# Kernel tuning notes

Hardware: AMD Instinct MI355X
Metric: run time of the kernel (lower is better)

## Reference

```python
import jax, jax.numpy as jnp
import numpy as np

# Per-channel block sizes (init arg). [0,1] rows are identity channels.
BLOCK_SIZES = np.array(
    [[0, 1]] * 2 + [[1, 1]] * 2 + [[2, 2]] * 4 + [[4, 4]] * 4 + [[3, 3]] * 4
)


def _groups():
    """Static grouping: unique non-identity block sizes -> channel index arrays."""
    out = []
    for b in np.unique(BLOCK_SIZES, axis=0):
        if 0 in b:
            continue  # identity channels: passed through untouched
        ch = np.where(np.all(BLOCK_SIZES == b, axis=1))[0]
        out.append(((int(b[0]), int(b[1])), ch))
    return out


GROUPS = _groups()


def setup_inputs() -> dict:
    key = jax.random.key(0)
    activation = jax.random.normal(key, (32, 16, 224, 224), dtype=jnp.float32)
    return {"activation": activation}


def reference(activation) -> jnp.ndarray:
    N, C, H, W = activation.shape
    relu_map = jnp.ones_like(activation)
    for (bh, bw), ch in GROUPS:
        cur = activation[:, ch]                      # [N, Cg, H, W] channel gather
        ph, pw = (-H) % bh, (-W) % bw                # pad to block multiples
        cur = jnp.pad(cur, ((0, 0), (0, 0), (0, ph), (0, pw)))
        Hp, Wp = H + ph, W + pw
        Cg = cur.shape[1]
        # space-to-depth block sum (sum sign == mean sign)
        s = cur.reshape(N, Cg, Hp // bh, bh, Wp // bw, bw).sum(axis=(3, 5))
        sign = (s >= 0).astype(activation.dtype)     # DReLU on block sum
        # broadcast sign back over each block (depth-to-space) and unpad
        m = jnp.broadcast_to(
            sign[:, :, :, None, :, None], (N, Cg, Hp // bh, bh, Wp // bw, bw)
        ).reshape(N, Cg, Hp, Wp)[:, :, :H, :W]
        relu_map = relu_map.at[:, ch].set(m)         # channel scatter
    # identity channels keep relu_map == 1, so a single multiply is faithful
    return activation * relu_map
```

## Files before the change

### kernel.cpp

```cpp
#include <hip/hip_runtime.h>

#define HW      224
#define PLANE   50176
#define NSTRIDE 802816

constexpr int A_BLOCKS = 6272;
constexpr int AB   = A_BLOCKS;
constexpr int ABC  = AB + 3136;
constexpr int ABCD = ABC + 1568;
constexpr int TOTAL_BLOCKS = ABCD + 3200;

__global__ __launch_bounds__(256) void blockrelu_kernel(
    const float* __restrict__ in, float* __restrict__ out) {
  const int bid = blockIdx.x;
  const int t = threadIdx.x;

  __shared__ float tile[9][228];
  __shared__ float maskL[3][76];

  if (bid < AB) {
    int tid = bid * 256 + t;
    int n = tid / PLANE;
    int r = tid - n * PLANE;
    int c = r / 12544;
    long off = (long)n * NSTRIDE + (long)r * 4;
    float4 v = *(const float4*)(in + off);
    if (c >= 2) {
      v.x = (v.x >= 0.f) ? v.x : 0.f;
      v.y = (v.y >= 0.f) ? v.y : 0.f;
      v.z = (v.z >= 0.f) ? v.z : 0.f;
      v.w = (v.w >= 0.f) ? v.w : 0.f;
    }
    *(float4*)(out + off) = v;
  } else if (bid < ABC) {
    int u = (bid - AB) * 256 + t;
    int n = u / 25088;
    int v2 = u - n * 25088;
    int c = 4 + v2 / 6272;
    int w2 = v2 % 6272;
    int brow = w2 / 56;
    int rcol = w2 - brow * 56;
    long base = (long)n * NSTRIDE + (long)c * PLANE + (long)(2 * brow) * HW + 4 * rcol;
    float4 a = *(const float4*)(in + base);
    float4 b = *(const float4*)(in + base + HW);
    float s0 = ((a.x + a.y) + b.x) + b.y;
    float s1 = ((a.z + a.w) + b.z) + b.w;
    if (s0 < 0.f) { a.x = 0.f; a.y = 0.f; b.x = 0.f; b.y = 0.f; }
    if (s1 < 0.f) { a.z = 0.f; a.w = 0.f; b.z = 0.f; b.w = 0.f; }
    *(float4*)(out + base) = a;
    *(float4*)(out + base + HW) = b;
  } else if (bid < ABCD) {
    int u = (bid - ABC) * 256 + t;
    int n = u / 12544;
    int v2 = u - n * 12544;
    int c = 8 + v2 / 3136;
    int w2 = v2 % 3136;
    int by = w2 / 56;
    int bx = w2 - by * 56;
    long base = (long)n * NSTRIDE + (long)c * PLANE + (long)(4 * by) * HW + 4 * bx;
    float4 r0 = *(const float4*)(in + base);
    float4 r1 = *(const float4*)(in + base + HW);
    float4 r2 = *(const float4*)(in + base + 2 * HW);
    float4 r3 = *(const float4*)(in + base + 3 * HW);
    float s = r0.x; s += r0.y; s += r0.z; s += r0.w;
    s += r1.x; s += r1.y; s += r1.z; s += r1.w;
    s += r2.x; s += r2.y; s += r2.z; s += r2.w;
    s += r3.x; s += r3.y; s += r3.z; s += r3.w;
    if (s < 0.f) {
      r0 = make_float4(0.f, 0.f, 0.f, 0.f);
      r1 = r0; r2 = r0; r3 = r0;
    }
    *(float4*)(out + base) = r0;
    *(float4*)(out + base + HW) = r1;
    *(float4*)(out + base + 2 * HW) = r2;
    *(float4*)(out + base + 3 * HW) = r3;
  } else {
    int wg = bid - ABCD;
    int p = wg / 25;
    int sg = wg - p * 25;
    int n = p >> 2;
    int c = 12 + (p & 3);
    int h0 = sg * 9;
    int rows = (224 - h0 >= 9) ? 9 : (224 - h0);
    long pbase = (long)n * NSTRIDE + (long)c * PLANE;

    for (int i = t; i < 9 * 228; i += 256) ((float*)tile)[i] = 0.f;
    __syncthreads();

    const int nvec = rows * 56;
    for (int idx = t; idx < nvec; idx += 256) {
      int r = idx / 56;
      int q = idx - r * 56;
      float4 v = *(const float4*)(in + pbase + (long)(h0 + r) * HW + q * 4);
      *(float4*)&tile[r][q * 4] = v;
    }
    __syncthreads();

    if (t < 225) {
      int br = t / 75;
      int bx = t - br * 75;
      int r0 = br * 3, c0 = bx * 3;
      float s = 0.f;
      #pragma unroll
      for (int i = 0; i < 3; ++i)
        #pragma unroll
        for (int j = 0; j < 3; ++j)
          s += tile[r0 + i][c0 + j];
      maskL[br][bx] = (s >= 0.f) ? 1.f : 0.f;
    }
    __syncthreads();

    for (int idx = t; idx < nvec; idx += 256) {
      int r = idx / 56;
      int q = idx - r * 56;
      int col = q * 4;
      float4 v = *(const float4*)&tile[r][col];
      int br = r / 3;
      v.x *= maskL[br][(col    ) / 3];
      v.y *= maskL[br][(col + 1) / 3];
      v.z *= maskL[br][(col + 2) / 3];
      v.w *= maskL[br][(col + 3) / 3];
      *(float4*)(out + pbase + (long)(h0 + r) * HW + col) = v;
    }
  }
}

extern "C" void kernel_launch(void* const* d_in, const int* in_sizes, int n_in,
                              void* d_out, int out_size, void* d_ws, size_t ws_size,
                              hipStream_t stream) {
  const float* act = (const float*)d_in[0];
  float* out = (float*)d_out;
  blockrelu_kernel<<<TOTAL_BLOCKS, 256, 0, stream>>>(act, out);
}
```

Measured before the change: 183.4 us.

## Compute 3x3 block channels in registers and reorder heavy work first

The 3x3-block channels no longer stage rows through shared memory with barriers. Each thread now loads a 3-row by 12-column patch as float4s, computes four block sums in registers and writes the masked values directly, with edge predicates for the 224 boundary. The block dispatch order is reversed so the heaviest per-block work (3x3, then 4x4, then 2x2) is scheduled first. The elementwise ReLU/identity section now processes two float4s per thread with half as many blocks. This removes the syncthreads and shared-memory traffic and should balance the tail, at the cost of more registers and 48-byte strided per-thread accesses that coalesce less well.

```diff
diff --git a/kernel.cpp b/kernel.cpp
--- a/kernel.cpp
+++ b/kernel.cpp
@@ -4,53 +4,89 @@
 #define PLANE   50176
 #define NSTRIDE 802816
 
-constexpr int A_BLOCKS = 6272;
-constexpr int AB   = A_BLOCKS;
-constexpr int ABC  = AB + 3136;
-constexpr int ABCD = ABC + 1568;
-constexpr int TOTAL_BLOCKS = ABCD + 3200;
+constexpr int D_END    = 713;
+constexpr int DC_END   = D_END + 1568;
+constexpr int DCB_END  = DC_END + 3136;
+constexpr int TOTAL_BLOCKS = DCB_END + 3136;
 
 __global__ __launch_bounds__(256) void blockrelu_kernel(
     const float* __restrict__ in, float* __restrict__ out) {
   const int bid = blockIdx.x;
   const int t = threadIdx.x;
 
-  __shared__ float tile[9][228];
-  __shared__ float maskL[3][76];
+  if (bid < D_END) {
+    int u = bid * 256 + t;
+    if (u < 182400) {
+      int p   = u / 1425;
+      int rem = u - p * 1425;
+      int br  = rem / 19;
+      int cu  = rem - br * 19;
+      int n = p >> 2;
+      int c = 12 + (p & 3);
+      const bool full = (cu < 18);
+      const bool r3   = (br < 74);
+      long base = (long)n * NSTRIDE + (long)c * PLANE + (long)(3 * br) * HW + 12 * cu;
 
-  if (bid < AB) {
-    int tid = bid * 256 + t;
-    int n = tid / PLANE;
-    int r = tid - n * PLANE;
-    int c = r / 12544;
-    long off = (long)n * NSTRIDE + (long)r * 4;
-    float4 v = *(const float4*)(in + off);
-    if (c >= 2) {
-      v.x = (v.x >= 0.f) ? v.x : 0.f;
-      v.y = (v.y >= 0.f) ? v.y : 0.f;
-      v.z = (v.z >= 0.f) ? v.z : 0.f;
-      v.w = (v.w >= 0.f) ? v.w : 0.f;
+      const float4 z4 = make_float4(0.f, 0.f, 0.f, 0.f);
+      float4 x00, x01, x02 = z4;
+      float4 x10, x11, x12 = z4;
+      float4 x20 = z4, x21 = z4, x22 = z4;
+      x00 = *(const float4*)(in + base);
+      x01 = *(const float4*)(in + base + 4);
+      if (full) x02 = *(const float4*)(in + base + 8);
+      x10 = *(const float4*)(in + base + HW);
+      x11 = *(const float4*)(in + base + HW + 4);
+      if (full) x12 = *(const float4*)(in + base + HW + 8);
+      if (r3) {
+        x20 = *(const float4*)(in + base + 2 * HW);
+        x21 = *(const float4*)(in + base + 2 * HW + 4);
+        if (full) x22 = *(const float4*)(in + base + 2 * HW + 8);
+      }
+
+      float s0, s1, s2, s3;
+      s0 = x00.x; s0 += x00.y; s0 += x00.z;
+      s0 += x10.x; s0 += x10.y; s0 += x10.z;
+      s0 += x20.x; s0 += x20.y; s0 += x20.z;
+
+      s1 = x00.w; s1 += x01.x; s1 += x01.y;
+      s1 += x10.w; s1 += x11.x; s1 += x11.y;
+      s1 += x20.w; s1 += x21.x; s1 += x21.y;
+
+      s2 = x01.z; s2 += x01.w; s2 += x02.x;
+      s2 += x11.z; s2 += x11.w; s2 += x12.x;
+      s2 += x21.z; s2 += x21.w; s2 += x22.x;
+
+      s3 = x02.y; s3 += x02.z; s3 += x02.w;
+      s3 += x12.y; s3 += x12.z; s3 += x12.w;
+      s3 += x22.y; s3 += x22.z; s3 += x22.w;
+
+      if (s0 < 0.f) { x00.x = x00.y = x00.z = 0.f;
+                      x10.x = x10.y = x10.z = 0.f;
+                      x20.x = x20.y = x20.z = 0.f; }
+      if (s1 < 0.f) { x00.w = x01.x = x01.y = 0.f;
+                      x10.w = x11.x = x11.y = 0.f;
+                      x20.w = x21.x = x21.y = 0.f; }
+      if (s2 < 0.f) { x01.z = x01.w = x02.x = 0.f;
+                      x11.z = x11.w = x12.x = 0.f;
+                      x21.z = x21.w = x22.x = 0.f; }
+      if (s3 < 0.f) { x02.y = x02.z = x02.w = 0.f;
+                      x12.y = x12.z = x12.w = 0.f;
+                      x22.y = x22.z = x22.w = 0.f; }
+
+      *(float4*)(out + base) = x00;
+      *(float4*)(out + base + 4) = x01;
+      if (full) *(float4*)(out + base + 8) = x02;
+      *(float4*)(out + base + HW) = x10;
+      *(float4*)(out + base + HW + 4) = x11;
+      if (full) *(float4*)(out + base + HW + 8) = x12;
+      if (r3) {
+        *(float4*)(out + base + 2 * HW) = x20;
+        *(float4*)(out + base + 2 * HW + 4) = x21;
+        if (full) *(float4*)(out + base + 2 * HW + 8) = x22;
+      }
     }
-    *(float4*)(out + off) = v;
-  } else if (bid < ABC) {
-    int u = (bid - AB) * 256 + t;
-    int n = u / 25088;
-    int v2 = u - n * 25088;
-    int c = 4 + v2 / 6272;
-    int w2 = v2 % 6272;
-    int brow = w2 / 56;
-    int rcol = w2 - brow * 56;
-    long base = (long)n * NSTRIDE + (long)c * PLANE + (long)(2 * brow) * HW + 4 * rcol;
-    float4 a = *(const float4*)(in + base);
-    float4 b = *(const float4*)(in + base + HW);
-    float s0 = ((a.x + a.y) + b.x) + b.y;
-    float s1 = ((a.z + a.w) + b.z) + b.w;
-    if (s0 < 0.f) { a.x = 0.f; a.y = 0.f; b.x = 0.f; b.y = 0.f; }
-    if (s1 < 0.f) { a.z = 0.f; a.w = 0.f; b.z = 0.f; b.w = 0.f; }
-    *(float4*)(out + base) = a;
-    *(float4*)(out + base + HW) = b;
-  } else if (bid < ABCD) {
-    int u = (bid - ABC) * 256 + t;
+  } else if (bid < DC_END) {
+    int u = (bid - D_END) * 256 + t;
     int n = u / 12544;
     int v2 = u - n * 12544;
     int c = 8 + v2 / 3136;
@@ -74,54 +110,50 @@
     *(float4*)(out + base + HW) = r1;
     *(float4*)(out + base + 2 * HW) = r2;
     *(float4*)(out + base + 3 * HW) = r3;
+  } else if (bid < DCB_END) {
+    int u = (bid - DC_END) * 256 + t;
+    int n = u / 25088;
+    int v2 = u - n * 25088;
+    int c = 4 + v2 / 6272;
+    int w2 = v2 % 6272;
+    int brow = w2 / 56;
+    int rcol = w2 - brow * 56;
+    long base = (long)n * NSTRIDE + (long)c * PLANE + (long)(2 * brow) * HW + 4 * rcol;
+    float4 a = *(const float4*)(in + base);
+    float4 b = *(const float4*)(in + base + HW);
+    float s0 = ((a.x + a.y) + b.x) + b.y;
+    float s1 = ((a.z + a.w) + b.z) + b.w;
+    if (s0 < 0.f) { a.x = 0.f; a.y = 0.f; b.x = 0.f; b.y = 0.f; }
+    if (s1 < 0.f) { a.z = 0.f; a.w = 0.f; b.z = 0.f; b.w = 0.f; }
+    *(float4*)(out + base) = a;
+    *(float4*)(out + base + HW) = b;
   } else {
-    int wg = bid - ABCD;
-    int p = wg / 25;
-    int sg = wg - p * 25;
-    int n = p >> 2;
-    int c = 12 + (p & 3);
-    int h0 = sg * 9;
-    int rows = (224 - h0 >= 9) ? 9 : (224 - h0);
-    long pbase = (long)n * NSTRIDE + (long)c * PLANE;
-
-    for (int i = t; i < 9 * 228; i += 256) ((float*)tile)[i] = 0.f;
-    __syncthreads();
-
-    const int nvec = rows * 56;
-    for (int idx = t; idx < nvec; idx += 256) {
-      int r = idx / 56;
-      int q = idx - r * 56;
-      float4 v = *(const float4*)(in + pbase + (long)(h0 + r) * HW + q * 4);
-      *(float4*)&tile[r][q * 4] = v;
+    int tid1 = (bid - DCB_END) * 512 + t;
+    int tid2 = tid1 + 256;
+    int n1 = tid1 / PLANE;
+    int r1 = tid1 - n1 * PLANE;
+    int c1 = r1 / 12544;
+    long off1 = (long)n1 * NSTRIDE + (long)r1 * 4;
+    int n2 = tid2 / PLANE;
+    int r2 = tid2 - n2 * PLANE;
+    int c2 = r2 / 12544;
+    long off2 = (long)n2 * NSTRIDE + (long)r2 * 4;
+    float4 v1 = *(const float4*)(in + off1);
+    float4 v2 = *(const float4*)(in + off2);
+    if (c1 >= 2) {
+      v1.x = (v1.x >= 0.f) ? v1.x : 0.f;
+      v1.y = (v1.y >= 0.f) ? v1.y : 0.f;
+      v1.z = (v1.z >= 0.f) ? v1.z : 0.f;
+      v1.w = (v1.w >= 0.f) ? v1.w : 0.f;
     }
-    __syncthreads();
-
-    if (t < 225) {
-      int br = t / 75;
-      int bx = t - br * 75;
-      int r0 = br * 3, c0 = bx * 3;
-      float s = 0.f;
-      #pragma unroll
-      for (int i = 0; i < 3; ++i)
-        #pragma unroll
-        for (int j = 0; j < 3; ++j)
-          s += tile[r0 + i][c0 + j];
-      maskL[br][bx] = (s >= 0.f) ? 1.f : 0.f;
+    if (c2 >= 2) {
+      v2.x = (v2.x >= 0.f) ? v2.x : 0.f;
+      v2.y = (v2.y >= 0.f) ? v2.y : 0.f;
+      v2.z = (v2.z >= 0.f) ? v2.z : 0.f;
+      v2.w = (v2.w >= 0.f) ? v2.w : 0.f;
     }
-    __syncthreads();
-
-    for (int idx = t; idx < nvec; idx += 256) {
-      int r = idx / 56;
-      int q = idx - r * 56;
-      int col = q * 4;
-      float4 v = *(const float4*)&tile[r][col];
-      int br = r / 3;
-      v.x *= maskL[br][(col    ) / 3];
-      v.y *= maskL[br][(col + 1) / 3];
-      v.z *= maskL[br][(col + 2) / 3];
-      v.w *= maskL[br][(col + 3) / 3];
-      *(float4*)(out + pbase + (long)(h0 + r) * HW + col) = v;
-    }
+    *(float4*)(out + off1) = v1;
+    *(float4*)(out + off2) = v2;
   }
 }
 
```

Result: no change. 185.0 us (+0.9%).
